# Kernel tuning notes

Measured on AMD Instinct MI355X. Metric: run time of the kernel, lower is better.

Reference implementation:

```python
import jax, jax.numpy as jnp
import numpy as np

B, T, N, E = 8, 80, 50000, 1600000
DT = 0.02  # integration time step (seconds)


def setup_inputs() -> dict:
    key = jax.random.key(0)
    ks = jax.random.split(key, 8)
    # stimulus over time: (batch, timesteps, n_nodes)
    x = jax.random.normal(ks[0], (B, T, N), dtype=jnp.float32)
    # node params (RestingPotential ~ N(0.5, 0.05); TimeConstant = 0.05)
    bias = 0.5 + 0.05 * jax.random.normal(ks[1], (N,), dtype=jnp.float32)
    time_const = jnp.full((N,), 0.05, dtype=jnp.float32)
    # edge params: sign in {-1,+1}, lognormal-ish counts, small non-negative strengths
    sign = jnp.where(jax.random.uniform(ks[2], (E,)) < 0.5, -1.0, 1.0).astype(jnp.float32)
    syn_count = jax.random.uniform(ks[3], (E,), dtype=jnp.float32, minval=0.5, maxval=5.0)
    syn_strength = jax.random.uniform(ks[4], (E,), dtype=jnp.float32, minval=0.0, maxval=0.02)
    source_indices = jax.random.randint(ks[5], (E,), 0, N, dtype=jnp.int32)
    target_indices = jax.random.randint(ks[6], (E,), 0, N, dtype=jnp.int32)
    return dict(x=x, bias=bias, time_const=time_const, sign=sign,
                syn_count=syn_count, syn_strength=syn_strength,
                source_indices=source_indices, target_indices=target_indices)


def reference(x, bias, time_const, sign, syn_count, syn_strength,
              source_indices, target_indices):
    """PPNeuronIGRSynapses dynamics with Euler integration.

    v_{t+1} = v_t + dt/max(tau, dt) * (-v_t + bias + scatter_add(w * relu(v_src)) + x_t)
    with w = sign * syn_count * clamp_nonneg(syn_strength).
    Returns activities of shape (B, T, N).
    """
    n_nodes = bias.shape[0]
    # derived edge weight (syn_strength clamped non-negative per clamp config)
    weight = sign * syn_count * jnp.maximum(syn_strength, 0.0)  # (E,)
    inv_tau = 1.0 / jnp.maximum(time_const, DT)                 # (N,)
    v0 = jnp.broadcast_to(bias, (x.shape[0], n_nodes))          # initial state = bias

    def step(v, x_t):
        # gather source activity across edges, relu activation, weight -> edge currents
        cur = weight * jnp.maximum(v[:, source_indices], 0.0)   # (B, E)
        # scatter-add edge currents into target nodes
        i_syn = jnp.zeros_like(v).at[:, target_indices].add(cur)  # (B, N)
        v_next = v + DT * inv_tau * (-v + bias + i_syn + x_t)
        return v_next, v_next

    _, vs = jax.lax.scan(step, v0, jnp.swapaxes(x, 0, 1))  # vs: (T, B, N)
    return jnp.swapaxes(vs, 0, 1)  # (B, T, N)
```

## Files before the change

kernel.cpp:

```cpp
#include <hip/hip_runtime.h>
#include <hip/hip_bf16.h>

#define NN 50000
#define NE 1600000
#define NB 8
#define NT 80
#define TN ((size_t)NT * NN)
#define DT_F 0.02f

#define LPN 8
#define KPRE 6

#define BKT_SHIFT 11
#define NBKT 25
#define NBKT_PAD 32
#define BKT_CAP 72000
#define ACHUNK 1024
#define BPB 64


__global__ void init_nodes_kernel(const float* __restrict__ bias,
                                  const float* __restrict__ tc,
                                  float* __restrict__ v0,
                                  ushort* __restrict__ r0,
                                  float* __restrict__ alpha,
                                  int* __restrict__ cnt,
                                  int* __restrict__ bucket_cursor) {
  int n = blockIdx.x * blockDim.x + threadIdx.x;
  if (n >= NN) return;
  float b = bias[n];
  __hip_bfloat16 rb = __float2bfloat16(fmaxf(b, 0.f));
  ushort rbu = *(ushort*)&rb;
#pragma unroll
  for (int j = 0; j < NB; ++j) {
    v0[(size_t)n * NB + j] = b;
    r0[(size_t)n * NB + j] = rbu;
  }
  alpha[n] = DT_F / fmaxf(tc[n], DT_F);
  cnt[n] = 0;
  if (n < NBKT_PAD) bucket_cursor[n] = 0;
}

__global__ void hist_kernel(const int* __restrict__ tgt, int* __restrict__ cnt) {
  int e = blockIdx.x * blockDim.x + threadIdx.x;
  if (e >= NE) return;
  atomicAdd(&cnt[tgt[e]], 1);
}

__global__ void fill_kernel(const int* __restrict__ src, const int* __restrict__ tgt,
                            const float* __restrict__ sgn, const float* __restrict__ syn_cnt,
                            const float* __restrict__ syn_str,
                            int* __restrict__ cursor,
                            int2* __restrict__ csr) {
  int e = blockIdx.x * blockDim.x + threadIdx.x;
  if (e >= NE) return;
  int t = tgt[e];
  float w = sgn[e] * syn_cnt[e] * fmaxf(syn_str[e], 0.f);
  int pos = atomicAdd(&cursor[t], 1);
  csr[pos] = make_int2(src[e] * (NB * 2), __float_as_int(w));
}

__global__ __launch_bounds__(256) void fillA_kernel(
    const int* __restrict__ src, const int* __restrict__ tgt,
    const float* __restrict__ sgn, const float* __restrict__ syn_cnt,
    const float* __restrict__ syn_str,
    int* __restrict__ node_cnt,
    int* __restrict__ bucket_cursor,
    unsigned long long* __restrict__ bkt) {
  __shared__ int bcnt[NBKT];
  __shared__ int bbase[NBKT];
  __shared__ int bpos[NBKT + 1];
  __shared__ unsigned long long stage[ACHUNK];
  __shared__ unsigned char stageb[ACHUNK];

  const int tid = threadIdx.x;
  const int base = blockIdx.x * ACHUNK;

  int b_[4], off_[4];
  unsigned long long ent_[4];
  bool val_[4];
#pragma unroll
  for (int k = 0; k < 4; ++k) {
    int e = base + k * 256 + tid;
    val_[k] = e < NE;
    b_[k] = 0;
    ent_[k] = 0;
    if (val_[k]) {
      int s = src[e];
      int t = tgt[e];
      float w = sgn[e] * syn_cnt[e] * fmaxf(syn_str[e], 0.f);
      atomicAdd(&node_cnt[t], 1);
      b_[k] = t >> BKT_SHIFT;
      unsigned int packed = (unsigned int)s | ((unsigned int)(t & ((1 << BKT_SHIFT) - 1)) << 16);
      ent_[k] = ((unsigned long long)(unsigned int)__float_as_int(w) << 32) | packed;
    }
  }

  if (tid < NBKT) bcnt[tid] = 0;
  __syncthreads();
#pragma unroll
  for (int k = 0; k < 4; ++k)
    if (val_[k]) off_[k] = atomicAdd(&bcnt[b_[k]], 1);
  __syncthreads();
  if (tid == 0) {
    int run = 0;
    for (int i = 0; i < NBKT; ++i) { bpos[i] = run; run += bcnt[i]; }
    bpos[NBKT] = run;
  }
  __syncthreads();
  if (tid < NBKT) bbase[tid] = atomicAdd(&bucket_cursor[tid], bcnt[tid]);
#pragma unroll
  for (int k = 0; k < 4; ++k) {
    if (val_[k]) {
      int slot = bpos[b_[k]] + off_[k];
      stage[slot] = ent_[k];
      stageb[slot] = (unsigned char)b_[k];
    }
  }
  __syncthreads();
  const int tot = bpos[NBKT];
  for (int i = tid; i < tot; i += 256) {
    int bb = stageb[i];
    int dst = bbase[bb] + (i - bpos[bb]);
    if (dst < BKT_CAP)
      bkt[(size_t)bb * BKT_CAP + dst] = stage[i];
  }
}

__global__ __launch_bounds__(256) void fillB_kernel(
    const unsigned long long* __restrict__ bkt,
    const int* __restrict__ bucket_cursor,
    int* __restrict__ cursor,
    int2* __restrict__ csr) {
  const int b = blockIdx.x & (NBKT_PAD - 1);
  if (b >= NBKT) return;
  const int j = blockIdx.x >> 5;
  const int count = bucket_cursor[b];
  const unsigned long long* mybkt = bkt + (size_t)b * BKT_CAP;
  for (int i = j * 256 + threadIdx.x; i < count; i += BPB * 256) {
    unsigned long long ent = mybkt[i];
    unsigned int packed = (unsigned int)ent;
    int w_bits = (int)(ent >> 32);
    int s = packed & 0xFFFF;
    int t = (b << BKT_SHIFT) + ((packed >> 16) & ((1 << BKT_SHIFT) - 1));
    int pos = atomicAdd(&cursor[t], 1);
    csr[pos] = make_int2(s * (NB * 2), w_bits);
  }
}

#define SCAN_BS 256
#define SCAN_NB ((NN + SCAN_BS - 1) / SCAN_BS)

__global__ __launch_bounds__(SCAN_BS) void scan1_kernel(
    const int* __restrict__ cnt, int* __restrict__ escan,
    int* __restrict__ partials) {
  __shared__ int buf[2][SCAN_BS];
  const int tid = threadIdx.x;
  const int i = blockIdx.x * SCAN_BS + tid;
  int v = (i < NN) ? cnt[i] : 0;
  int sel = 0;
  buf[0][tid] = v;
  __syncthreads();
#pragma unroll
  for (int off = 1; off < SCAN_BS; off <<= 1) {
    int s = buf[sel][tid];
    if (tid >= off) s += buf[sel][tid - off];
    buf[sel ^ 1][tid] = s;
    sel ^= 1;
    __syncthreads();
  }
  int incl = buf[sel][tid];
  if (i < NN) escan[i] = incl - v;
  if (tid == SCAN_BS - 1) partials[blockIdx.x] = incl;
}

__global__ __launch_bounds__(SCAN_BS) void scan2_kernel(
    int* __restrict__ partials, int* __restrict__ row_ptr) {
  __shared__ int buf[2][SCAN_BS];
  const int tid = threadIdx.x;
  int v = (tid < SCAN_NB) ? partials[tid] : 0;
  int sel = 0;
  buf[0][tid] = v;
  __syncthreads();
#pragma unroll
  for (int off = 1; off < SCAN_BS; off <<= 1) {
    int s = buf[sel][tid];
    if (tid >= off) s += buf[sel][tid - off];
    buf[sel ^ 1][tid] = s;
    sel ^= 1;
    __syncthreads();
  }
  int incl = buf[sel][tid];
  if (tid < SCAN_NB) partials[tid] = incl - v;
  if (tid == SCAN_BS - 1) row_ptr[NN] = incl;
}

__global__ __launch_bounds__(SCAN_BS) void scan3_kernel(
    const int* __restrict__ escan, const int* __restrict__ partials,
    int* __restrict__ row_ptr, int* __restrict__ cursor) {
  const int i = blockIdx.x * SCAN_BS + threadIdx.x;
  if (i >= NN) return;
  int r = escan[i] + partials[blockIdx.x];
  row_ptr[i] = r;
  cursor[i] = r;
}

__global__ __launch_bounds__(256) void step1_kernel(
    const int* __restrict__ row_ptr,
    const int2* __restrict__ csr,
    const float* __restrict__ v_old,
    const ushort* __restrict__ r_old,
    float* __restrict__ v_new,
    ushort* __restrict__ r_new,
    const float* __restrict__ x_t,
    const float* __restrict__ bias,
    const float* __restrict__ alpha,
    float* __restrict__ out_t) {
  int gid = blockIdx.x * blockDim.x + threadIdx.x;
  int node = gid >> 3;
  int lane = gid & 7;
  if (node >= NN) return;

  int e0 = row_ptr[node];
  int e1 = row_ptr[node + 1];
  int mybase = e0 + lane;
  int rem = e1 - mybase;
  int cnt = rem > 0 ? ((rem + LPN - 1) >> 3) : 0;

  float a = alpha[node];
  float bs = bias[node];
  size_t idx = (size_t)node * NB + lane;
  size_t boff = (size_t)lane * TN + node;
  float v = v_old[idx];
  float xv = __builtin_nontemporal_load(&x_t[boff]);

  int soff[KPRE];
  float wk[KPRE];
#pragma unroll
  for (int k = 0; k < KPRE; ++k) {
    int2 c = (k < cnt) ? csr[mybase + (k << 3)] : make_int2(0, 0);
    soff[k] = c.x;
    wk[k] = __int_as_float(c.y);
  }

  uint4 rv[KPRE];
#pragma unroll
  for (int k = 0; k < KPRE; ++k) {
    if (k < cnt)
      rv[k] = *(const uint4*)((const char*)r_old + soff[k]);
    else
      rv[k] = make_uint4(0, 0, 0, 0);
  }

  float acc[NB];
#pragma unroll
  for (int j = 0; j < NB; ++j) acc[j] = 0.f;

#pragma unroll
  for (int k = 0; k < KPRE; ++k) {
    float w = wk[k];
    acc[0] += w * __uint_as_float(rv[k].x << 16);
    acc[1] += w * __uint_as_float(rv[k].x & 0xffff0000u);
    acc[2] += w * __uint_as_float(rv[k].y << 16);
    acc[3] += w * __uint_as_float(rv[k].y & 0xffff0000u);
    acc[4] += w * __uint_as_float(rv[k].z << 16);
    acc[5] += w * __uint_as_float(rv[k].z & 0xffff0000u);
    acc[6] += w * __uint_as_float(rv[k].w << 16);
    acc[7] += w * __uint_as_float(rv[k].w & 0xffff0000u);
  }

  for (int e = mybase + (KPRE << 3); e < e1; e += LPN) {
    int2 c = csr[e];
    uint4 r8 = *(const uint4*)((const char*)r_old + c.x);
    float w = __int_as_float(c.y);
    acc[0] += w * __uint_as_float(r8.x << 16);
    acc[1] += w * __uint_as_float(r8.x & 0xffff0000u);
    acc[2] += w * __uint_as_float(r8.y << 16);
    acc[3] += w * __uint_as_float(r8.y & 0xffff0000u);
    acc[4] += w * __uint_as_float(r8.z << 16);
    acc[5] += w * __uint_as_float(r8.z & 0xffff0000u);
    acc[6] += w * __uint_as_float(r8.w << 16);
    acc[7] += w * __uint_as_float(r8.w & 0xffff0000u);
  }

#pragma unroll
  for (int off = 4; off; off >>= 1) {
#pragma unroll
    for (int j = 0; j < NB; ++j) {
      float t = __shfl_xor(acc[j], off);
      acc[j] = (((lane ^ j) & off) == 0) ? acc[j] + t : acc[j];
    }
  }
  float r = acc[0];
#pragma unroll
  for (int j = 1; j < NB; ++j) r = (lane == j) ? acc[j] : r;

  float vn = v + a * (bs - v + r + xv);
  v_new[idx] = vn;
  __hip_bfloat16 rh = __float2bfloat16(fmaxf(vn, 0.f));
  r_new[idx] = *(ushort*)&rh;
  __builtin_nontemporal_store(vn, &out_t[boff]);
}


extern "C" void kernel_launch(void* const* d_in, const int* in_sizes, int n_in,
                              void* d_out, int out_size, void* d_ws, size_t ws_size,
                              hipStream_t stream) {
  const float* x        = (const float*)d_in[0];
  const float* bias     = (const float*)d_in[1];
  const float* tc       = (const float*)d_in[2];
  const float* sgn      = (const float*)d_in[3];
  const float* syn_cnt  = (const float*)d_in[4];
  const float* syn_str  = (const float*)d_in[5];
  const int*   src      = (const int*)d_in[6];
  const int*   tgt      = (const int*)d_in[7];
  float* out = (float*)d_out;

  char* p = (char*)d_ws;
  auto take = [&p](size_t bytes) {
    char* r = p;
    p += (bytes + 255) & ~(size_t)255;
    return (void*)r;
  };
  float*  v_a      = (float*)take((size_t)NN * NB * sizeof(float));
  float*  v_b      = (float*)take((size_t)NN * NB * sizeof(float));
  ushort* r_a      = (ushort*)take((size_t)NN * NB * sizeof(ushort));
  ushort* r_b      = (ushort*)take((size_t)NN * NB * sizeof(ushort));
  float*  alpha    = (float*)take((size_t)NN * sizeof(float));
  int*    row_ptr  = (int*)take(((size_t)NN + 1) * sizeof(int));
  int*    cnt      = (int*)take((size_t)NN * sizeof(int));
  int*    cursor   = (int*)take((size_t)NN * sizeof(int));
  int*    escan    = (int*)take((size_t)NN * sizeof(int));
  int*    partials = (int*)take((size_t)SCAN_NB * sizeof(int));
  int*    bcur     = (int*)take((size_t)NBKT_PAD * sizeof(int));
  int2*   csr      = (int2*)take((size_t)NE * sizeof(int2));
  char*   end_base = p;
  unsigned long long* bkt =
      (unsigned long long*)take((size_t)NBKT * BKT_CAP * sizeof(unsigned long long));
  const bool use_bucketed = ((size_t)(p - (char*)d_ws) <= ws_size);
  (void)end_base;

  init_nodes_kernel<<<(NN + 255) / 256, 256, 0, stream>>>(bias, tc, v_a, r_a,
                                                          alpha, cnt, bcur);
  if (use_bucketed) {
    fillA_kernel<<<(NE + ACHUNK - 1) / ACHUNK, 256, 0, stream>>>(
        src, tgt, sgn, syn_cnt, syn_str, cnt, bcur, bkt);
    scan1_kernel<<<SCAN_NB, SCAN_BS, 0, stream>>>(cnt, escan, partials);
    scan2_kernel<<<1, SCAN_BS, 0, stream>>>(partials, row_ptr);
    scan3_kernel<<<SCAN_NB, SCAN_BS, 0, stream>>>(escan, partials, row_ptr, cursor);
    fillB_kernel<<<NBKT_PAD * BPB, 256, 0, stream>>>(bkt, bcur, cursor, csr);
  } else {
    hist_kernel<<<(NE + 255) / 256, 256, 0, stream>>>(tgt, cnt);
    scan1_kernel<<<SCAN_NB, SCAN_BS, 0, stream>>>(cnt, escan, partials);
    scan2_kernel<<<1, SCAN_BS, 0, stream>>>(partials, row_ptr);
    scan3_kernel<<<SCAN_NB, SCAN_BS, 0, stream>>>(escan, partials, row_ptr, cursor);
    fill_kernel<<<(NE + 255) / 256, 256, 0, stream>>>(src, tgt, sgn, syn_cnt,
                                                      syn_str, cursor, csr);
  }

  const int blocks = (NN * LPN + 255) / 256;
  const float* vin = v_a;
  float* vout = v_b;
  const ushort* rin = r_a;
  ushort* rout = r_b;
  for (int t = 0; t < NT; ++t) {
    step1_kernel<<<blocks, 256, 0, stream>>>(
        row_ptr, csr, vin, rin, vout, rout,
        x + (size_t)t * NN, bias, alpha, out + (size_t)t * NN);
    float* tv = (float*)vin; vin = vout; vout = tv;
    ushort* tr = (ushort*)rin; rin = rout; rout = tr;
  }
}
```

Baseline: 1.146 ms.

## Pack CSR edges into 32 bits with bf16 weights and read state from output

Each CSR entry shrinks from an int2 holding a source byte offset and an fp32 weight to one 32-bit word holding a 16-bit source index and a bf16 weight, which halves edge-stream traffic in every timestep. The separate fp32 state double buffer is removed; each step reads the previous voltage from the previous output slice, and out stores become normal stores so they stay cached for the next step. The fillA chunk size is also doubled. Rounding weights to bf16 lowers precision, and the 16-bit source index only works because the node count stays below 65536.

```diff
diff --git a/kernel.cpp b/kernel.cpp
--- a/kernel.cpp
+++ b/kernel.cpp
@@ -15,13 +15,12 @@
 #define NBKT 25
 #define NBKT_PAD 32
 #define BKT_CAP 72000
-#define ACHUNK 1024
+#define ACHUNK 2048
 #define BPB 64
 
 
 __global__ void init_nodes_kernel(const float* __restrict__ bias,
                                   const float* __restrict__ tc,
-                                  float* __restrict__ v0,
                                   ushort* __restrict__ r0,
                                   float* __restrict__ alpha,
                                   int* __restrict__ cnt,
@@ -32,10 +31,7 @@
   __hip_bfloat16 rb = __float2bfloat16(fmaxf(b, 0.f));
   ushort rbu = *(ushort*)&rb;
 #pragma unroll
-  for (int j = 0; j < NB; ++j) {
-    v0[(size_t)n * NB + j] = b;
-    r0[(size_t)n * NB + j] = rbu;
-  }
+  for (int j = 0; j < NB; ++j) r0[(size_t)n * NB + j] = rbu;
   alpha[n] = DT_F / fmaxf(tc[n], DT_F);
   cnt[n] = 0;
   if (n < NBKT_PAD) bucket_cursor[n] = 0;
@@ -51,13 +47,15 @@
                             const float* __restrict__ sgn, const float* __restrict__ syn_cnt,
                             const float* __restrict__ syn_str,
                             int* __restrict__ cursor,
-                            int2* __restrict__ csr) {
+                            unsigned int* __restrict__ csr) {
   int e = blockIdx.x * blockDim.x + threadIdx.x;
   if (e >= NE) return;
   int t = tgt[e];
   float w = sgn[e] * syn_cnt[e] * fmaxf(syn_str[e], 0.f);
+  __hip_bfloat16 wh = __float2bfloat16(w);
+  unsigned int wb = *(ushort*)&wh;
   int pos = atomicAdd(&cursor[t], 1);
-  csr[pos] = make_int2(src[e] * (NB * 2), __float_as_int(w));
+  csr[pos] = (unsigned int)src[e] | (wb << 16);
 }
 
 __global__ __launch_bounds__(256) void fillA_kernel(
@@ -75,12 +73,13 @@
 
   const int tid = threadIdx.x;
   const int base = blockIdx.x * ACHUNK;
-
-  int b_[4], off_[4];
-  unsigned long long ent_[4];
-  bool val_[4];
-#pragma unroll
-  for (int k = 0; k < 4; ++k) {
+#define EPT (ACHUNK / 256)
+
+  int b_[EPT], off_[EPT];
+  unsigned long long ent_[EPT];
+  bool val_[EPT];
+#pragma unroll
+  for (int k = 0; k < EPT; ++k) {
     int e = base + k * 256 + tid;
     val_[k] = e < NE;
     b_[k] = 0;
@@ -99,7 +98,7 @@
   if (tid < NBKT) bcnt[tid] = 0;
   __syncthreads();
 #pragma unroll
-  for (int k = 0; k < 4; ++k)
+  for (int k = 0; k < EPT; ++k)
     if (val_[k]) off_[k] = atomicAdd(&bcnt[b_[k]], 1);
   __syncthreads();
   if (tid == 0) {
@@ -110,7 +109,7 @@
   __syncthreads();
   if (tid < NBKT) bbase[tid] = atomicAdd(&bucket_cursor[tid], bcnt[tid]);
 #pragma unroll
-  for (int k = 0; k < 4; ++k) {
+  for (int k = 0; k < EPT; ++k) {
     if (val_[k]) {
       int slot = bpos[b_[k]] + off_[k];
       stage[slot] = ent_[k];
@@ -125,13 +124,14 @@
     if (dst < BKT_CAP)
       bkt[(size_t)bb * BKT_CAP + dst] = stage[i];
   }
+#undef EPT
 }
 
 __global__ __launch_bounds__(256) void fillB_kernel(
     const unsigned long long* __restrict__ bkt,
     const int* __restrict__ bucket_cursor,
     int* __restrict__ cursor,
-    int2* __restrict__ csr) {
+    unsigned int* __restrict__ csr) {
   const int b = blockIdx.x & (NBKT_PAD - 1);
   if (b >= NBKT) return;
   const int j = blockIdx.x >> 5;
@@ -140,11 +140,13 @@
   for (int i = j * 256 + threadIdx.x; i < count; i += BPB * 256) {
     unsigned long long ent = mybkt[i];
     unsigned int packed = (unsigned int)ent;
-    int w_bits = (int)(ent >> 32);
-    int s = packed & 0xFFFF;
+    float w = __int_as_float((int)(ent >> 32));
+    unsigned int s = packed & 0xFFFF;
     int t = (b << BKT_SHIFT) + ((packed >> 16) & ((1 << BKT_SHIFT) - 1));
+    __hip_bfloat16 wh = __float2bfloat16(w);
+    unsigned int wb = *(ushort*)&wh;
     int pos = atomicAdd(&cursor[t], 1);
-    csr[pos] = make_int2(s * (NB * 2), w_bits);
+    csr[pos] = s | (wb << 16);
   }
 }
 
@@ -207,15 +209,15 @@
 
 __global__ __launch_bounds__(256) void step1_kernel(
     const int* __restrict__ row_ptr,
-    const int2* __restrict__ csr,
-    const float* __restrict__ v_old,
+    const unsigned int* __restrict__ csr,
     const ushort* __restrict__ r_old,
-    float* __restrict__ v_new,
     ushort* __restrict__ r_new,
     const float* __restrict__ x_t,
+    const float* __restrict__ vprev,
     const float* __restrict__ bias,
     const float* __restrict__ alpha,
-    float* __restrict__ out_t) {
+    float* __restrict__ out_t,
+    int first) {
   int gid = blockIdx.x * blockDim.x + threadIdx.x;
   int node = gid >> 3;
   int lane = gid & 7;
@@ -231,16 +233,17 @@
   float bs = bias[node];
   size_t idx = (size_t)node * NB + lane;
   size_t boff = (size_t)lane * TN + node;
-  float v = v_old[idx];
   float xv = __builtin_nontemporal_load(&x_t[boff]);
+  float v = bs;
+  if (!first) v = vprev[boff];
 
   int soff[KPRE];
   float wk[KPRE];
 #pragma unroll
   for (int k = 0; k < KPRE; ++k) {
-    int2 c = (k < cnt) ? csr[mybase + (k << 3)] : make_int2(0, 0);
-    soff[k] = c.x;
-    wk[k] = __int_as_float(c.y);
+    unsigned int c = (k < cnt) ? csr[mybase + (k << 3)] : 0u;
+    soff[k] = (int)(c & 0xFFFFu) << 4;
+    wk[k] = __uint_as_float(c & 0xFFFF0000u);
   }
 
   uint4 rv[KPRE];
@@ -270,9 +273,9 @@
   }
 
   for (int e = mybase + (KPRE << 3); e < e1; e += LPN) {
-    int2 c = csr[e];
-    uint4 r8 = *(const uint4*)((const char*)r_old + c.x);
-    float w = __int_as_float(c.y);
+    unsigned int c = csr[e];
+    uint4 r8 = *(const uint4*)((const char*)r_old + ((size_t)(c & 0xFFFFu) << 4));
+    float w = __uint_as_float(c & 0xFFFF0000u);
     acc[0] += w * __uint_as_float(r8.x << 16);
     acc[1] += w * __uint_as_float(r8.x & 0xffff0000u);
     acc[2] += w * __uint_as_float(r8.y << 16);
@@ -296,10 +299,9 @@
   for (int j = 1; j < NB; ++j) r = (lane == j) ? acc[j] : r;
 
   float vn = v + a * (bs - v + r + xv);
-  v_new[idx] = vn;
   __hip_bfloat16 rh = __float2bfloat16(fmaxf(vn, 0.f));
   r_new[idx] = *(ushort*)&rh;
-  __builtin_nontemporal_store(vn, &out_t[boff]);
+  out_t[boff] = vn;
 }
 
 
@@ -322,8 +324,6 @@
     p += (bytes + 255) & ~(size_t)255;
     return (void*)r;
   };
-  float*  v_a      = (float*)take((size_t)NN * NB * sizeof(float));
-  float*  v_b      = (float*)take((size_t)NN * NB * sizeof(float));
   ushort* r_a      = (ushort*)take((size_t)NN * NB * sizeof(ushort));
   ushort* r_b      = (ushort*)take((size_t)NN * NB * sizeof(ushort));
   float*  alpha    = (float*)take((size_t)NN * sizeof(float));
@@ -333,14 +333,12 @@
   int*    escan    = (int*)take((size_t)NN * sizeof(int));
   int*    partials = (int*)take((size_t)SCAN_NB * sizeof(int));
   int*    bcur     = (int*)take((size_t)NBKT_PAD * sizeof(int));
-  int2*   csr      = (int2*)take((size_t)NE * sizeof(int2));
-  char*   end_base = p;
+  unsigned int* csr = (unsigned int*)take((size_t)NE * sizeof(unsigned int));
   unsigned long long* bkt =
       (unsigned long long*)take((size_t)NBKT * BKT_CAP * sizeof(unsigned long long));
   const bool use_bucketed = ((size_t)(p - (char*)d_ws) <= ws_size);
-  (void)end_base;
-
-  init_nodes_kernel<<<(NN + 255) / 256, 256, 0, stream>>>(bias, tc, v_a, r_a,
+
+  init_nodes_kernel<<<(NN + 255) / 256, 256, 0, stream>>>(bias, tc, r_a,
                                                           alpha, cnt, bcur);
   if (use_bucketed) {
     fillA_kernel<<<(NE + ACHUNK - 1) / ACHUNK, 256, 0, stream>>>(
@@ -359,15 +357,16 @@
   }
 
   const int blocks = (NN * LPN + 255) / 256;
-  const float* vin = v_a;
-  float* vout = v_b;
   const ushort* rin = r_a;
   ushort* rout = r_b;
   for (int t = 0; t < NT; ++t) {
     step1_kernel<<<blocks, 256, 0, stream>>>(
-        row_ptr, csr, vin, rin, vout, rout,
-        x + (size_t)t * NN, bias, alpha, out + (size_t)t * NN);
-    float* tv = (float*)vin; vin = vout; vout = tv;
+        row_ptr, csr, rin, rout,
+        x + (size_t)t * NN,
+        out + (size_t)(t > 0 ? t - 1 : 0) * NN,
+        bias, alpha,
+        out + (size_t)t * NN,
+        t == 0 ? 1 : 0);
     ushort* tr = (ushort*)rin; rin = rout; rout = tr;
   }
 }
```

New measurement: 1.123 ms. 1.02x faster.
